# Optimization experiments

Hardware: AMD Instinct MI355X
Metric: run time of the kernel (lower is better)

## Reference

```python
import jax, jax.numpy as jnp
import numpy as np

BN = 1024      # B*N voxel groups
M = 32         # points per voxel
D_MODEL = 128
D_POINTS = 64


def _mlp(x, w1, b1, w2, b2):
    # Linear -> ReLU -> Linear (torch nn.Sequential equivalent)
    return jax.nn.relu(x @ w1 + b1) @ w2 + b2


def setup_inputs() -> dict:
    key = jax.random.key(0)
    ks = jax.random.split(key, 16)
    def lin(k, din, dout):
        return (jax.random.normal(k, (din, dout), jnp.float32) / np.sqrt(din)).astype(jnp.float32)
    inp = {}
    inp["pv_xyz"] = jax.random.normal(ks[0], (BN, M, 3), jnp.float32)
    inp["features"] = jax.random.normal(ks[1], (BN, M, D_POINTS), jnp.float32)
    i = 2
    for name, din in [("alpha", 3), ("beta", 3), ("delta", 3), ("epsilon", D_MODEL), ("omega", D_POINTS)]:
        inp[f"{name}_w1"] = lin(ks[i], din, D_MODEL); i += 1
        inp[f"{name}_b1"] = jnp.zeros((D_MODEL,), jnp.float32)
        inp[f"{name}_w2"] = lin(ks[i], D_MODEL, D_MODEL); i += 1
        inp[f"{name}_b2"] = jnp.zeros((D_MODEL,), jnp.float32)
    return inp


def reference(pv_xyz, features,
              alpha_w1, alpha_b1, alpha_w2, alpha_b2,
              beta_w1, beta_b1, beta_w2, beta_b2,
              delta_w1, delta_b1, delta_w2, delta_b2,
              epsilon_w1, epsilon_b1, epsilon_w2, epsilon_b2,
              omega_w1, omega_b1, omega_w2, omega_b2):
    # abs relative position: [BN, M, M, 3]
    dist = jnp.abs(pv_xyz[:, :, None, :] - pv_xyz[:, None, :, :])
    pij = _mlp(dist, delta_w1, delta_b1, delta_w2, delta_b2)          # [BN,M,M,D]
    q = _mlp(pv_xyz, alpha_w1, alpha_b1, alpha_w2, alpha_b2)          # [BN,M,D]
    k = _mlp(pv_xyz, beta_w1, beta_b1, beta_w2, beta_b2)              # [BN,M,D]
    v = _mlp(features, omega_w1, omega_b1, omega_w2, omega_b2)        # [BN,M,D]
    scale = jnp.float32(1.0 / np.sqrt(D_MODEL))
    w = _mlp((q[:, :, None, :] - k[:, None, :, :] + pij) * scale,
             epsilon_w1, epsilon_b1, epsilon_w2, epsilon_b2)          # [BN,M,M,D]
    wij = jax.nn.softmax(w, axis=-2)                                  # softmax over key axis
    # torch.einsum('bmmf,bmf->bmf', wij, v): repeated index -> diagonal of wij
    midx = jnp.arange(wij.shape[1])
    res = wij[:, midx, midx, :] * v                                   # [BN,M,D]
    return jnp.concatenate([res, features], axis=-1)                  # [BN,M,D+C]
```

## Files before the change

### kernel.cpp

```cpp
#include <hip/hip_runtime.h>
#include <hip/hip_bf16.h>
#include <cstdint>
#include <cstddef>


#define SCALE 0.08838834764831843f
#define LOG2E 1.4426950408889634f

typedef __bf16 bf16x8 __attribute__((ext_vector_type(8)));
typedef float f32x16 __attribute__((ext_vector_type(16)));

__device__ __forceinline__ ushort f2b(float f){
  __hip_bfloat16 h = __float2bfloat16(f);
  return __builtin_bit_cast(ushort, h);
}
__device__ __forceinline__ float b2f(uint32_t s){
  union { uint32_t u; float f; } x; x.u = s << 16; return x.f;
}
__device__ __forceinline__ float blo(uint32_t u){
  union { uint32_t x; float f; } v; v.x = u << 16; return v.f;
}
__device__ __forceinline__ float bhi(uint32_t u){
  union { uint32_t x; float f; } v; v.x = u & 0xffff0000u; return v.f;
}
__device__ __forceinline__ uint32_t pk2(float a, float b){
  union { __hip_bfloat162 h2; uint32_t u; } x;
  x.h2.x = __float2bfloat16(a); x.h2.y = __float2bfloat16(b);
  return x.u;
}
__device__ __forceinline__ f32x16 MFMA(uint4 a, uint4 b, f32x16 c){
  return __builtin_amdgcn_mfma_f32_32x32x16_bf16(
      __builtin_bit_cast(bf16x8, a), __builtin_bit_cast(bf16x8, b), c, 0, 0, 0);
}

__global__ __launch_bounds__(256) void k_pre(
    const float* __restrict__ A2, const float* __restrict__ B2, const float* __restrict__ D2,
    const float* __restrict__ E1, const float* __restrict__ E2,
    const float* __restrict__ O1, const float* __restrict__ O2,
    const float* __restrict__ ab2, const float* __restrict__ bb2, const float* __restrict__ db2,
    const float* __restrict__ eb1,
    const float* __restrict__ D1, const float* __restrict__ db1,
    ushort* __restrict__ aep, ushort* __restrict__ bep, ushort* __restrict__ gtp,
    ushort* __restrict__ e2p, ushort* __restrict__ o2p, ushort* __restrict__ o1t,
    ushort* __restrict__ d1p, float* __restrict__ c0)
{
  const int bid = blockIdx.x, tid = threadIdx.x;
  if (bid < 192){
    const float* W = (bid < 64) ? A2 : (bid < 128) ? B2 : D2;
    ushort* dst    = (bid < 64) ? aep : (bid < 128) ? bep : gtp;
    int flat = (bid & 63)*256 + tid;
    int co = flat >> 10, rem = flat & 1023, h = rem >> 3, i = rem & 7;
    int r = co*8 + i;
    float acc = 0.f;
    for (int t = 0; t < 128; ++t) acc = fmaf(W[r*128 + t], E1[t*128 + h], acc);
    dst[(co*128 + h)*8 + i] = f2b(acc * SCALE);
  } else if (bid < 256){
    int flat = (bid - 192)*256 + tid;
    int co = flat >> 10, rem = flat & 1023, d = rem >> 3, i = rem & 7;
    e2p[(co*128 + d)*8 + i] = f2b(E2[(co*8 + i)*128 + d] * LOG2E);
  } else if (bid < 320){
    int flat = (bid - 256)*256 + tid;
    int co = flat >> 10, rem = flat & 1023, d = rem >> 3, i = rem & 7;
    o2p[(co*128 + d)*8 + i] = f2b(O2[(co*8 + i)*128 + d]);
  } else if (bid < 352){
    int flat = (bid - 320)*256 + tid;
    int fo = flat >> 10, rem = flat & 1023, o = rem >> 3, e = rem & 7;
    o1t[(fo*128 + o)*8 + e] = f2b(O1[(fo*8 + e)*128 + o]);
  } else if (bid < 360){
    int flat = (bid - 352)*256 + tid;
    int koct = flat >> 10, cd = (flat >> 3) & 127, e = flat & 7;
    float val = 0.f;
    if (koct == 0){
      if (e < 3) val = D1[e*128 + cd];
      else if (e == 3) val = db1[cd];
    }
    d1p[flat] = f2b(val);
  } else {
    if (tid < 128){
      float acc = 0.f;
      for (int t = 0; t < 128; ++t) acc = fmaf(ab2[t] - bb2[t] + db2[t], E1[t*128 + tid], acc);
      c0[tid] = acc * SCALE + eb1[tid];
    }
  }
}

__device__ __forceinline__ void gemm64x128(const ushort (*sa)[64][8], const ushort (*sw)[128][8],
                                           int w, int l31, int hl, int p0,
                                           const float* __restrict__ bias,
                                           ushort* __restrict__ dst)
{
  const int rw = w >> 1, ctb = (w & 1) * 2;
  f32x16 acc0, acc1;
#pragma unroll
  for (int r = 0; r < 16; ++r){ acc0[r] = 0.f; acc1[r] = 0.f; }
#pragma unroll
  for (int kk = 0; kk < 8; ++kk){
    uint4 a  = *(const uint4*)&sa[2*kk + hl][32*rw + l31][0];
    uint4 b0 = *(const uint4*)&sw[2*kk + hl][32*ctb + l31][0];
    uint4 b1 = *(const uint4*)&sw[2*kk + hl][32*(ctb+1) + l31][0];
    acc0 = MFMA(a, b0, acc0);
    acc1 = MFMA(a, b1, acc1);
  }
#pragma unroll
  for (int t = 0; t < 2; ++t){
    const f32x16 acc = t ? acc1 : acc0;
    const int d = 32*(ctb + t) + l31;
    const float bv = bias ? bias[d] : 0.f;
#pragma unroll
    for (int r = 0; r < 16; ++r){
      int row = 32*rw + (r & 3) + 8*(r >> 2) + 4*hl;
      dst[(size_t)(p0 + row)*128 + d] = f2b(acc[r] + bv);
    }
  }
}

__global__ __launch_bounds__(256, 2) void k_point(
    const float* __restrict__ pv, const float* __restrict__ feat,
    const float* __restrict__ A1, const float* __restrict__ ab1,
    const float* __restrict__ B1, const float* __restrict__ bb1,
    const float* __restrict__ ob1, const float* __restrict__ ob2,
    const float* __restrict__ c0,
    const uint4* __restrict__ aep, const uint4* __restrict__ bep,
    const uint4* __restrict__ o1t, const uint4* __restrict__ o2p,
    ushort* __restrict__ qe_ws, ushort* __restrict__ ke_ws, ushort* __restrict__ v_ws,
    float* __restrict__ out)
{
  __shared__ ushort sW[16][128][8];
  __shared__ ushort sA[16][64][8];
  __shared__ ushort sF[8][64][8];
  __shared__ float  sLw[3][128];
  __shared__ float  sLb[128];
  __shared__ float  sLb2[128];

  const int tid = threadIdx.x;
  const int p0  = blockIdx.x * 64;
  const int w = tid >> 6, lane = tid & 63, l31 = lane & 31, hl = lane >> 5;

  for (int idx = tid; idx < 64*16; idx += 256){
    int p = idx >> 4, k4 = idx & 15;
    float4 f = ((const float4*)(feat + (size_t)(p0 + p)*64))[k4];
    ((float4*)(out + (size_t)(p0 + p)*192 + 128))[k4] = f;
  }

  for (int idx = tid; idx < 2048; idx += 256) ((uint4*)sW)[idx] = aep[idx];
  for (int idx = tid; idx < 384; idx += 256) ((float*)sLw)[idx] = A1[idx];
  if (tid < 128) sLb[tid] = ab1[tid];
  __syncthreads();
  {
    int p = tid & 63, ob = tid >> 6;
    float x0 = pv[(size_t)(p0+p)*3+0], x1 = pv[(size_t)(p0+p)*3+1], x2 = pv[(size_t)(p0+p)*3+2];
#pragma unroll
    for (int it = 0; it < 4; ++it){
      int oct = ob + 4*it;
      float h[8];
#pragma unroll
      for (int e = 0; e < 8; ++e){
        int cd = oct*8 + e;
        float t = fmaf(x0, sLw[0][cd], fmaf(x1, sLw[1][cd], fmaf(x2, sLw[2][cd], sLb[cd])));
        h[e] = fmaxf(t, 0.f);
      }
      uint4 u; u.x = pk2(h[0],h[1]); u.y = pk2(h[2],h[3]); u.z = pk2(h[4],h[5]); u.w = pk2(h[6],h[7]);
      *(uint4*)&sA[oct][p][0] = u;
    }
  }
  __syncthreads();
  gemm64x128(sA, sW, w, l31, hl, p0, c0, qe_ws);
  __syncthreads();

  for (int idx = tid; idx < 2048; idx += 256) ((uint4*)sW)[idx] = bep[idx];
  for (int idx = tid; idx < 384; idx += 256) ((float*)sLw)[idx] = B1[idx];
  if (tid < 128) sLb[tid] = bb1[tid];
  __syncthreads();
  {
    int p = tid & 63, ob = tid >> 6;
    float x0 = pv[(size_t)(p0+p)*3+0], x1 = pv[(size_t)(p0+p)*3+1], x2 = pv[(size_t)(p0+p)*3+2];
#pragma unroll
    for (int it = 0; it < 4; ++it){
      int oct = ob + 4*it;
      float h[8];
#pragma unroll
      for (int e = 0; e < 8; ++e){
        int cd = oct*8 + e;
        float t = fmaf(x0, sLw[0][cd], fmaf(x1, sLw[1][cd], fmaf(x2, sLw[2][cd], sLb[cd])));
        h[e] = fmaxf(t, 0.f);
      }
      uint4 u; u.x = pk2(h[0],h[1]); u.y = pk2(h[2],h[3]); u.z = pk2(h[4],h[5]); u.w = pk2(h[6],h[7]);
      *(uint4*)&sA[oct][p][0] = u;
    }
  }
  __syncthreads();
  gemm64x128(sA, sW, w, l31, hl, p0, nullptr, ke_ws);
  __syncthreads();

  for (int idx = tid; idx < 512; idx += 256){
    int p = idx & 63, fo = idx >> 6;
    const float* fp = feat + (size_t)(p0 + p)*64 + 8*fo;
    float4 f0 = ((const float4*)fp)[0], f1 = ((const float4*)fp)[1];
    uint4 u; u.x = pk2(f0.x,f0.y); u.y = pk2(f0.z,f0.w); u.z = pk2(f1.x,f1.y); u.w = pk2(f1.z,f1.w);
    *(uint4*)&sF[fo][p][0] = u;
  }
  for (int idx = tid; idx < 1024; idx += 256) ((uint4*)sW)[idx] = o1t[idx];
  if (tid < 128) sLb[tid] = ob1[tid];
  __syncthreads();
  {
    f32x16 acc0, acc1;
#pragma unroll
    for (int r = 0; r < 16; ++r){ acc0[r] = 0.f; acc1[r] = 0.f; }
#pragma unroll
    for (int kk = 0; kk < 4; ++kk){
      uint4 a  = *(const uint4*)&sW[2*kk + hl][32*w + l31][0];
      uint4 b0 = *(const uint4*)&sF[2*kk + hl][l31][0];
      uint4 b1 = *(const uint4*)&sF[2*kk + hl][32 + l31][0];
      acc0 = MFMA(a, b0, acc0);
      acc1 = MFMA(a, b1, acc1);
    }
#pragma unroll
    for (int t = 0; t < 2; ++t){
      const f32x16 acc = t ? acc1 : acc0;
      const int pt = 32*t + l31;
#pragma unroll
      for (int q = 0; q < 4; ++q){
        int o0 = 32*w + 8*q + 4*hl;
        float z0 = fmaxf(acc[4*q+0] + sLb[o0+0], 0.f);
        float z1 = fmaxf(acc[4*q+1] + sLb[o0+1], 0.f);
        float z2 = fmaxf(acc[4*q+2] + sLb[o0+2], 0.f);
        float z3 = fmaxf(acc[4*q+3] + sLb[o0+3], 0.f);
        uint2 u; u.x = pk2(z0, z1); u.y = pk2(z2, z3);
        *(uint2*)&sA[4*w + q][pt][4*hl] = u;
      }
    }
  }
  __syncthreads();

  for (int idx = tid; idx < 2048; idx += 256) ((uint4*)sW)[idx] = o2p[idx];
  if (tid < 128) sLb2[tid] = ob2[tid];
  __syncthreads();
  {
    const int rw = w >> 1, ctb = (w & 1) * 2;
    f32x16 acc0, acc1;
#pragma unroll
    for (int r = 0; r < 16; ++r){ acc0[r] = 0.f; acc1[r] = 0.f; }
#pragma unroll
    for (int kk = 0; kk < 8; ++kk){
      uint4 a  = *(const uint4*)&sA[2*kk + hl][32*rw + l31][0];
      uint4 b0 = *(const uint4*)&sW[2*kk + hl][32*ctb + l31][0];
      uint4 b1 = *(const uint4*)&sW[2*kk + hl][32*(ctb+1) + l31][0];
      acc0 = MFMA(a, b0, acc0);
      acc1 = MFMA(a, b1, acc1);
    }
#pragma unroll
    for (int t = 0; t < 2; ++t){
      const f32x16 acc = t ? acc1 : acc0;
      const int d = 32*(ctb + t) + l31;
      const float bias = sLb2[d];
#pragma unroll
      for (int r = 0; r < 16; ++r){
        int row = 32*rw + (r & 3) + 8*(r >> 2) + 4*hl;
        v_ws[(size_t)(p0 + row)*128 + d] = f2b(acc[r] + bias);
      }
    }
  }
}

__global__ __launch_bounds__(256, 3) void k_main(
    const float* __restrict__ pv,
    const ushort* __restrict__ qe_ws, const ushort* __restrict__ ke_ws, const ushort* __restrict__ v_ws,
    const uint4* __restrict__ gtp, const uint4* __restrict__ e2p, const uint4* __restrict__ d1p,
    float* __restrict__ out)
{
  __shared__ ushort sHDE[16][128][8];
  __shared__ float  sQE[16][128];
  __shared__ float  sXYZ[32][3];

  const int tid = threadIdx.x;
  const int b   = blockIdx.x >> 1;
  const int ch0 = (blockIdx.x & 1) * 4;
  const int w = tid >> 6, lane = tid & 63, l31 = lane & 31, hl = lane >> 5;

  for (int idx = tid; idx < 96; idx += 256) ((float*)sXYZ)[idx] = pv[(size_t)b*96 + idx];
  for (int idx = tid; idx < 512; idx += 256){
    int il = idx >> 5, sl = idx & 31;
    uint2 qu = ((const uint2*)qe_ws)[(size_t)(b*32 + 4*ch0 + il)*32 + sl];
    float4 o; o.x = blo(qu.x); o.y = bhi(qu.x); o.z = blo(qu.y); o.w = bhi(qu.y);
    ((float4*)&sQE[il][0])[sl] = o;
  }

  float kreg[16];
  {
    const ushort* kp = ke_ws + (size_t)(b*32 + l31)*128 + 32*w + 4*hl;
#pragma unroll
    for (int q = 0; q < 4; ++q){
      uint2 ku = *(const uint2*)(kp + 8*q);
      kreg[4*q+0] = blo(ku.x); kreg[4*q+1] = bhi(ku.x);
      kreg[4*q+2] = blo(ku.y); kreg[4*q+3] = bhi(ku.y);
    }
  }
  uint4 wG[8], wE[8];
#pragma unroll
  for (int kk = 0; kk < 8; ++kk){
    wG[kk] = gtp[(2*kk + hl)*128 + 32*w + l31];
    wE[kk] = e2p[(2*kk + hl)*128 + 32*w + l31];
  }
  uint4 wD = d1p[hl*128 + 32*w + l31];

  f32x16 ZERO;
#pragma unroll
  for (int r = 0; r < 16; ++r) ZERO[r] = 0.f;
  __syncthreads();

  const float xj0 = sXYZ[l31][0], xj1 = sXYZ[l31][1], xj2 = sXYZ[l31][2];

#pragma unroll
  for (int cc = 0; cc < 4; ++cc){
    const int c = ch0 + cc;

    f32x16 accD[4];
#pragma unroll
    for (int ct = 0; ct < 4; ++ct){
      const int i = 4*c + ct;
      float dx = fabsf(sXYZ[i][0] - xj0);
      float dy = fabsf(sXYZ[i][1] - xj1);
      float dz = fabsf(sXYZ[i][2] - xj2);
      uint4 bD; bD.x = pk2(dx, dy); bD.y = pk2(dz, 1.0f); bD.z = 0u; bD.w = 0u;
      accD[ct] = MFMA(wD, bD, ZERO);
    }
#pragma unroll
    for (int ct = 0; ct < 4; ++ct){
#pragma unroll
      for (int q = 0; q < 4; ++q){
        uint2 o;
        o.x = pk2(fmaxf(accD[ct][4*q+0],0.f), fmaxf(accD[ct][4*q+1],0.f));
        o.y = pk2(fmaxf(accD[ct][4*q+2],0.f), fmaxf(accD[ct][4*q+3],0.f));
        *(uint2*)&sHDE[4*w + q][32*ct + l31][4*hl] = o;
      }
    }
    __syncthreads();

    f32x16 acc1[4];
#pragma unroll
    for (int ct = 0; ct < 4; ++ct){
      const int il = 4*cc + ct;
#pragma unroll
      for (int q = 0; q < 4; ++q){
        float4 qv = *(const float4*)&sQE[il][32*w + 4*hl + 8*q];
        acc1[ct][4*q+0] = qv.x - kreg[4*q+0];
        acc1[ct][4*q+1] = qv.y - kreg[4*q+1];
        acc1[ct][4*q+2] = qv.z - kreg[4*q+2];
        acc1[ct][4*q+3] = qv.w - kreg[4*q+3];
      }
    }
#pragma unroll
    for (int kk = 0; kk < 8; ++kk){
      uint4 a = wG[kk];
#pragma unroll
      for (int ct = 0; ct < 4; ++ct){
        uint4 bu = *(const uint4*)&sHDE[2*kk + hl][32*ct + l31][0];
        acc1[ct] = MFMA(a, bu, acc1[ct]);
      }
    }
    __syncthreads();

#pragma unroll
    for (int ct = 0; ct < 4; ++ct){
#pragma unroll
      for (int q = 0; q < 4; ++q){
        uint2 o;
        o.x = pk2(fmaxf(acc1[ct][4*q+0],0.f), fmaxf(acc1[ct][4*q+1],0.f));
        o.y = pk2(fmaxf(acc1[ct][4*q+2],0.f), fmaxf(acc1[ct][4*q+3],0.f));
        *(uint2*)&sHDE[4*w + q][32*ct + l31][4*hl] = o;
      }
    }
    __syncthreads();

    float vv[4];
#pragma unroll
    for (int rt = 0; rt < 4; ++rt)
      vv[rt] = b2f((uint32_t)v_ws[(size_t)(b*32 + 4*c + rt)*128 + 32*w + l31]);

    f32x16 acc2[4];
#pragma unroll
    for (int kk = 0; kk < 8; ++kk){
      uint4 bfrag = wE[kk];
#pragma unroll
      for (int rt = 0; rt < 4; ++rt){
        uint4 au = *(const uint4*)&sHDE[2*kk + hl][32*rt + l31][0];
        acc2[rt] = MFMA(au, bfrag, kk ? acc2[rt] : ZERO);
      }
    }
    __syncthreads();

    const int g = (c >> 1) & 3;
    const int hls = c & 1;
#pragma unroll
    for (int rt = 0; rt < 4; ++rt){
      float e[16];
#pragma unroll
      for (int r = 0; r < 16; ++r) e[r] = __builtin_amdgcn_exp2f(acc2[rt][r]);
      float s01 = e[0]+e[1],   s23 = e[2]+e[3],   s45 = e[4]+e[5],   s67 = e[6]+e[7];
      float s89 = e[8]+e[9],   sab = e[10]+e[11], scd = e[12]+e[13], sef = e[14]+e[15];
      float s = ((s01+s23)+(s45+s67)) + ((s89+sab)+(scd+sef));
      s += __shfl_xor(s, 32);
      float num = (g == 0) ? e[rt] : (g == 1) ? e[rt+4] : (g == 2) ? e[rt+8] : e[rt+12];
      if (hl == hls){
        out[(size_t)(b*32 + 4*c + rt)*192 + 32*w + l31] = num * __builtin_amdgcn_rcpf(s) * vv[rt];
      }
    }
  }
}

static constexpr size_t OFF_AEP = 0;
static constexpr size_t OFF_BEP = 32768;
static constexpr size_t OFF_GTP = 65536;
static constexpr size_t OFF_E2P = 98304;
static constexpr size_t OFF_O1T = 131072;
static constexpr size_t OFF_O2P = 147456;
static constexpr size_t OFF_C0  = 180224;
static constexpr size_t OFF_D1P = 180736;
static constexpr size_t OFF_QE  = 184832;
static constexpr size_t OFF_KE  = OFF_QE + (size_t)32768*128*2;
static constexpr size_t OFF_V   = OFF_KE + (size_t)32768*128*2;

extern "C" void kernel_launch(void* const* d_in, const int* in_sizes, int n_in,
                              void* d_out, int out_size, void* d_ws, size_t ws_size,
                              hipStream_t stream)
{
  (void)in_sizes; (void)n_in; (void)out_size; (void)ws_size;
  const float* pv   = (const float*)d_in[0];
  const float* feat = (const float*)d_in[1];
  const float* A1 = (const float*)d_in[2];  const float* ab1 = (const float*)d_in[3];
  const float* A2 = (const float*)d_in[4];  const float* ab2 = (const float*)d_in[5];
  const float* B1 = (const float*)d_in[6];  const float* bb1 = (const float*)d_in[7];
  const float* B2 = (const float*)d_in[8];  const float* bb2 = (const float*)d_in[9];
  const float* D1 = (const float*)d_in[10]; const float* db1 = (const float*)d_in[11];
  const float* D2 = (const float*)d_in[12]; const float* db2 = (const float*)d_in[13];
  const float* E1 = (const float*)d_in[14]; const float* eb1 = (const float*)d_in[15];
  const float* E2 = (const float*)d_in[16];
  const float* O1 = (const float*)d_in[18]; const float* ob1 = (const float*)d_in[19];
  const float* O2 = (const float*)d_in[20]; const float* ob2 = (const float*)d_in[21];

  char* ws = (char*)d_ws;
  ushort* aep = (ushort*)(ws + OFF_AEP);
  ushort* bep = (ushort*)(ws + OFF_BEP);
  ushort* gtp = (ushort*)(ws + OFF_GTP);
  ushort* e2p = (ushort*)(ws + OFF_E2P);
  ushort* o1t = (ushort*)(ws + OFF_O1T);
  ushort* o2p = (ushort*)(ws + OFF_O2P);
  float*  c0  = (float*)(ws + OFF_C0);
  ushort* d1p = (ushort*)(ws + OFF_D1P);
  ushort* qe  = (ushort*)(ws + OFF_QE);
  ushort* ke  = (ushort*)(ws + OFF_KE);
  ushort* vv  = (ushort*)(ws + OFF_V);
  float* out = (float*)d_out;

  hipLaunchKernelGGL(k_pre, dim3(361), dim3(256), 0, stream,
                     A2, B2, D2, E1, E2, O1, O2, ab2, bb2, db2, eb1, D1, db1,
                     aep, bep, gtp, e2p, o2p, o1t, d1p, c0);
  hipLaunchKernelGGL(k_point, dim3(512), dim3(256), 0, stream,
                     pv, feat, A1, ab1, B1, bb1, ob1, ob2, c0,
                     (const uint4*)aep, (const uint4*)bep, (const uint4*)o1t, (const uint4*)o2p,
                     qe, ke, vv, out);
  hipLaunchKernelGGL(k_main, dim3(2048), dim3(256), 0, stream,
                     pv, qe, ke, vv, (const uint4*)gtp, (const uint4*)e2p, (const uint4*)d1p,
                     out);
}
```

Before: 118.7 us.

## Keep MLP intermediates in registers via permlane swaps instead of LDS round-trips

Restructures k_main so each wave owns two query rows at a time. The MFMA accumulator-to-operand layout conversion now happens in registers with permlane32_swap, replacing the shared-memory staging of hidden activations and its block-wide barriers. Weights G and E are moved from per-lane registers into LDS, the grid is halved to one block per voxel group, and the occupancy hint drops from 3 to 2. The cost is many more LDS weight reads per MFMA and higher register pressure, traded for removing all in-loop __syncthreads.

Result: no change. 120.1 us (+1.2%).

```diff
diff --git a/kernel.cpp b/kernel.cpp
--- a/kernel.cpp
+++ b/kernel.cpp
@@ -9,6 +9,7 @@
 
 typedef __bf16 bf16x8 __attribute__((ext_vector_type(8)));
 typedef float f32x16 __attribute__((ext_vector_type(16)));
+typedef unsigned int u32x2 __attribute__((ext_vector_type(2)));
 
 __device__ __forceinline__ ushort f2b(float f){
   __hip_bfloat16 h = __float2bfloat16(f);
@@ -31,6 +32,33 @@
 __device__ __forceinline__ f32x16 MFMA(uint4 a, uint4 b, f32x16 c){
   return __builtin_amdgcn_mfma_f32_32x32x16_bf16(
       __builtin_bit_cast(bf16x8, a), __builtin_bit_cast(bf16x8, b), c, 0, 0, 0);
+}
+
+__device__ __forceinline__ uint2 pswap(uint32_t a, uint32_t b){
+#if __has_builtin(__builtin_amdgcn_permlane32_swap)
+  u32x2 r = __builtin_amdgcn_permlane32_swap(a, b, false, false);
+  uint2 o; o.x = r[0]; o.y = r[1]; return o;
+#else
+  uint32_t am = (uint32_t)__shfl_xor((int)a, 32);
+  uint32_t bm = (uint32_t)__shfl_xor((int)b, 32);
+  bool hi = (threadIdx.x & 32) != 0;
+  uint2 o; o.x = hi ? bm : a; o.y = hi ? b : am; return o;
+#endif
+}
+
+__device__ __forceinline__ void packswap(const f32x16 c, uint4& f0, uint4& f1){
+  uint32_t p01 = pk2(fmaxf(c[0],0.f),  fmaxf(c[1],0.f));
+  uint32_t p23 = pk2(fmaxf(c[2],0.f),  fmaxf(c[3],0.f));
+  uint32_t p45 = pk2(fmaxf(c[4],0.f),  fmaxf(c[5],0.f));
+  uint32_t p67 = pk2(fmaxf(c[6],0.f),  fmaxf(c[7],0.f));
+  uint32_t p89 = pk2(fmaxf(c[8],0.f),  fmaxf(c[9],0.f));
+  uint32_t pab = pk2(fmaxf(c[10],0.f), fmaxf(c[11],0.f));
+  uint32_t pcd = pk2(fmaxf(c[12],0.f), fmaxf(c[13],0.f));
+  uint32_t pef = pk2(fmaxf(c[14],0.f), fmaxf(c[15],0.f));
+  uint2 s0 = pswap(p01, p45), s1 = pswap(p23, p67);
+  uint2 s2 = pswap(p89, pcd), s3 = pswap(pab, pef);
+  f0.x = s0.x; f0.y = s1.x; f0.z = s0.y; f0.w = s1.y;
+  f1.x = s2.x; f1.y = s3.x; f1.z = s2.y; f1.w = s3.y;
 }
 
 __global__ __launch_bounds__(256) void k_pre(
@@ -262,147 +290,119 @@
   }
 }
 
-__global__ __launch_bounds__(256, 3) void k_main(
+__global__ __launch_bounds__(256, 2) void k_main(
     const float* __restrict__ pv,
     const ushort* __restrict__ qe_ws, const ushort* __restrict__ ke_ws, const ushort* __restrict__ v_ws,
     const uint4* __restrict__ gtp, const uint4* __restrict__ e2p, const uint4* __restrict__ d1p,
     float* __restrict__ out)
 {
-  __shared__ ushort sHDE[16][128][8];
-  __shared__ float  sQE[16][128];
-  __shared__ float  sXYZ[32][3];
+  __shared__ uint4 sG[2048];
+  __shared__ uint4 sE[2048];
+  __shared__ uint2 sK[1024];
+  __shared__ float sXYZ[32][3];
 
   const int tid = threadIdx.x;
-  const int b   = blockIdx.x >> 1;
-  const int ch0 = (blockIdx.x & 1) * 4;
+  const int b = blockIdx.x;
   const int w = tid >> 6, lane = tid & 63, l31 = lane & 31, hl = lane >> 5;
 
+  for (int idx = tid; idx < 2048; idx += 256){ sG[idx] = gtp[idx]; sE[idx] = e2p[idx]; }
+  for (int idx = tid; idx < 1024; idx += 256){
+    int j = idx & 31, rest = idx >> 5;
+    int khl = rest & 1, slot = rest >> 1;
+    int h0 = 32*(slot >> 2) + 8*(slot & 3) + 4*khl;
+    sK[idx] = *(const uint2*)(ke_ws + (size_t)(b*32 + j)*128 + h0);
+  }
   for (int idx = tid; idx < 96; idx += 256) ((float*)sXYZ)[idx] = pv[(size_t)b*96 + idx];
-  for (int idx = tid; idx < 512; idx += 256){
-    int il = idx >> 5, sl = idx & 31;
-    uint2 qu = ((const uint2*)qe_ws)[(size_t)(b*32 + 4*ch0 + il)*32 + sl];
-    float4 o; o.x = blo(qu.x); o.y = bhi(qu.x); o.z = blo(qu.y); o.w = bhi(qu.y);
-    ((float4*)&sQE[il][0])[sl] = o;
-  }
-
-  float kreg[16];
-  {
-    const ushort* kp = ke_ws + (size_t)(b*32 + l31)*128 + 32*w + 4*hl;
-#pragma unroll
-    for (int q = 0; q < 4; ++q){
-      uint2 ku = *(const uint2*)(kp + 8*q);
-      kreg[4*q+0] = blo(ku.x); kreg[4*q+1] = bhi(ku.x);
-      kreg[4*q+2] = blo(ku.y); kreg[4*q+3] = bhi(ku.y);
-    }
-  }
-  uint4 wG[8], wE[8];
-#pragma unroll
-  for (int kk = 0; kk < 8; ++kk){
-    wG[kk] = gtp[(2*kk + hl)*128 + 32*w + l31];
-    wE[kk] = e2p[(2*kk + hl)*128 + 32*w + l31];
-  }
-  uint4 wD = d1p[hl*128 + 32*w + l31];
-
+
+  uint4 wD[4];
+#pragma unroll
+  for (int t = 0; t < 4; ++t) wD[t] = d1p[hl*128 + 32*t + l31];
   f32x16 ZERO;
 #pragma unroll
   for (int r = 0; r < 16; ++r) ZERO[r] = 0.f;
   __syncthreads();
 
   const float xj0 = sXYZ[l31][0], xj1 = sXYZ[l31][1], xj2 = sXYZ[l31][2];
-
-#pragma unroll
-  for (int cc = 0; cc < 4; ++cc){
-    const int c = ch0 + cc;
-
-    f32x16 accD[4];
-#pragma unroll
-    for (int ct = 0; ct < 4; ++ct){
-      const int i = 4*c + ct;
-      float dx = fabsf(sXYZ[i][0] - xj0);
-      float dy = fabsf(sXYZ[i][1] - xj1);
-      float dz = fabsf(sXYZ[i][2] - xj2);
-      uint4 bD; bD.x = pk2(dx, dy); bD.y = pk2(dz, 1.0f); bD.z = 0u; bD.w = 0u;
-      accD[ct] = MFMA(wD, bD, ZERO);
-    }
-#pragma unroll
-    for (int ct = 0; ct < 4; ++ct){
+  const ushort* qbase = qe_ws + (size_t)b*32*128;
+
+#pragma unroll
+  for (int pp = 0; pp < 4; ++pp){
+    const int i0 = 8*w + 2*pp, i1 = i0 + 1;
+
+    uint4 bDa, bDb;
+    {
+      float a0 = sXYZ[i0][0], a1 = sXYZ[i0][1], a2 = sXYZ[i0][2];
+      float c0_ = sXYZ[i1][0], c1_ = sXYZ[i1][1], c2_ = sXYZ[i1][2];
+      bDa.x = pk2(fabsf(a0-xj0), fabsf(a1-xj1)); bDa.y = pk2(fabsf(a2-xj2), 1.0f);
+      bDa.z = 0u; bDa.w = 0u;
+      bDb.x = pk2(fabsf(c0_-xj0), fabsf(c1_-xj1)); bDb.y = pk2(fabsf(c2_-xj2), 1.0f);
+      bDb.z = 0u; bDb.w = 0u;
+    }
+
+    uint4 hdA[8], hdB[8];
+#pragma unroll
+    for (int t = 0; t < 4; ++t){
+      f32x16 ca = MFMA(wD[t], bDa, ZERO);
+      f32x16 cb = MFMA(wD[t], bDb, ZERO);
+      packswap(ca, hdA[2*t], hdA[2*t+1]);
+      packswap(cb, hdB[2*t], hdB[2*t+1]);
+    }
+
+    uint4 heA[8], heB[8];
+#pragma unroll
+    for (int t = 0; t < 4; ++t){
+      f32x16 aA, aB;
 #pragma unroll
       for (int q = 0; q < 4; ++q){
-        uint2 o;
-        o.x = pk2(fmaxf(accD[ct][4*q+0],0.f), fmaxf(accD[ct][4*q+1],0.f));
-        o.y = pk2(fmaxf(accD[ct][4*q+2],0.f), fmaxf(accD[ct][4*q+3],0.f));
-        *(uint2*)&sHDE[4*w + q][32*ct + l31][4*hl] = o;
-      }
-    }
-    __syncthreads();
-
-    f32x16 acc1[4];
-#pragma unroll
-    for (int ct = 0; ct < 4; ++ct){
-      const int il = 4*cc + ct;
-#pragma unroll
-      for (int q = 0; q < 4; ++q){
-        float4 qv = *(const float4*)&sQE[il][32*w + 4*hl + 8*q];
-        acc1[ct][4*q+0] = qv.x - kreg[4*q+0];
-        acc1[ct][4*q+1] = qv.y - kreg[4*q+1];
-        acc1[ct][4*q+2] = qv.z - kreg[4*q+2];
-        acc1[ct][4*q+3] = qv.w - kreg[4*q+3];
-      }
-    }
-#pragma unroll
-    for (int kk = 0; kk < 8; ++kk){
-      uint4 a = wG[kk];
-#pragma unroll
-      for (int ct = 0; ct < 4; ++ct){
-        uint4 bu = *(const uint4*)&sHDE[2*kk + hl][32*ct + l31][0];
-        acc1[ct] = MFMA(a, bu, acc1[ct]);
-      }
-    }
-    __syncthreads();
-
-#pragma unroll
-    for (int ct = 0; ct < 4; ++ct){
-#pragma unroll
-      for (int q = 0; q < 4; ++q){
-        uint2 o;
-        o.x = pk2(fmaxf(acc1[ct][4*q+0],0.f), fmaxf(acc1[ct][4*q+1],0.f));
-        o.y = pk2(fmaxf(acc1[ct][4*q+2],0.f), fmaxf(acc1[ct][4*q+3],0.f));
-        *(uint2*)&sHDE[4*w + q][32*ct + l31][4*hl] = o;
-      }
-    }
-    __syncthreads();
-
-    float vv[4];
-#pragma unroll
-    for (int rt = 0; rt < 4; ++rt)
-      vv[rt] = b2f((uint32_t)v_ws[(size_t)(b*32 + 4*c + rt)*128 + 32*w + l31]);
-
-    f32x16 acc2[4];
-#pragma unroll
-    for (int kk = 0; kk < 8; ++kk){
-      uint4 bfrag = wE[kk];
-#pragma unroll
-      for (int rt = 0; rt < 4; ++rt){
-        uint4 au = *(const uint4*)&sHDE[2*kk + hl][32*rt + l31][0];
-        acc2[rt] = MFMA(au, bfrag, kk ? acc2[rt] : ZERO);
-      }
-    }
-    __syncthreads();
-
-    const int g = (c >> 1) & 3;
-    const int hls = c & 1;
-#pragma unroll
-    for (int rt = 0; rt < 4; ++rt){
-      float e[16];
-#pragma unroll
-      for (int r = 0; r < 16; ++r) e[r] = __builtin_amdgcn_exp2f(acc2[rt][r]);
-      float s01 = e[0]+e[1],   s23 = e[2]+e[3],   s45 = e[4]+e[5],   s67 = e[6]+e[7];
-      float s89 = e[8]+e[9],   sab = e[10]+e[11], scd = e[12]+e[13], sef = e[14]+e[15];
-      float s = ((s01+s23)+(s45+s67)) + ((s89+sab)+(scd+sef));
-      s += __shfl_xor(s, 32);
-      float num = (g == 0) ? e[rt] : (g == 1) ? e[rt+4] : (g == 2) ? e[rt+8] : e[rt+12];
-      if (hl == hls){
-        out[(size_t)(b*32 + 4*c + rt)*192 + 32*w + l31] = num * __builtin_amdgcn_rcpf(s) * vv[rt];
+        uint2 kq = sK[((t*4 + q)*2 + hl)*32 + l31];
+        uint2 qa = *(const uint2*)(qbase + (size_t)i0*128 + 32*t + 8*q + 4*hl);
+        uint2 qb = *(const uint2*)(qbase + (size_t)i1*128 + 32*t + 8*q + 4*hl);
+        float k0 = blo(kq.x), k1 = bhi(kq.x), k2 = blo(kq.y), k3 = bhi(kq.y);
+        aA[4*q+0] = blo(qa.x) - k0; aA[4*q+1] = bhi(qa.x) - k1;
+        aA[4*q+2] = blo(qa.y) - k2; aA[4*q+3] = bhi(qa.y) - k3;
+        aB[4*q+0] = blo(qb.x) - k0; aB[4*q+1] = bhi(qb.x) - k1;
+        aB[4*q+2] = blo(qb.y) - k2; aB[4*q+3] = bhi(qb.y) - k3;
+      }
+#pragma unroll
+      for (int kk = 0; kk < 8; ++kk){
+        uint4 wg = sG[(2*kk + hl)*128 + 32*t + l31];
+        aA = MFMA(wg, hdA[kk], aA);
+        aB = MFMA(wg, hdB[kk], aB);
+      }
+      packswap(aA, heA[2*t], heA[2*t+1]);
+      packswap(aB, heB[2*t], heB[2*t+1]);
+    }
+
+    const int rl   = (2*pp) & 3;
+    const int hsel = pp >> 1;
+#pragma unroll
+    for (int t = 0; t < 4; ++t){
+      float va = b2f((uint32_t)v_ws[(size_t)(b*32 + i0)*128 + 32*t + l31]);
+      float vb = b2f((uint32_t)v_ws[(size_t)(b*32 + i1)*128 + 32*t + l31]);
+      f32x16 cA, cB;
+#pragma unroll
+      for (int kk = 0; kk < 8; ++kk){
+        uint4 we = sE[(2*kk + hl)*128 + 32*t + l31];
+        cA = MFMA(heA[kk], we, kk ? cA : ZERO);
+        cB = MFMA(heB[kk], we, kk ? cB : ZERO);
+      }
+#pragma unroll
+      for (int r = 0; r < 16; ++r) cA[r] = __builtin_amdgcn_exp2f(cA[r]);
+#pragma unroll
+      for (int r = 0; r < 16; ++r) cB[r] = __builtin_amdgcn_exp2f(cB[r]);
+      float sA = ((cA[0]+cA[1])+(cA[2]+cA[3])) + ((cA[4]+cA[5])+(cA[6]+cA[7]))
+               + ((cA[8]+cA[9])+(cA[10]+cA[11])) + ((cA[12]+cA[13])+(cA[14]+cA[15]));
+      float sB = ((cB[0]+cB[1])+(cB[2]+cB[3])) + ((cB[4]+cB[5])+(cB[6]+cB[7]))
+               + ((cB[8]+cB[9])+(cB[10]+cB[11])) + ((cB[12]+cB[13])+(cB[14]+cB[15]));
+      uint2 swA = pswap(__builtin_bit_cast(uint32_t, sA), __builtin_bit_cast(uint32_t, sA));
+      uint2 swB = pswap(__builtin_bit_cast(uint32_t, sB), __builtin_bit_cast(uint32_t, sB));
+      float sAt = __builtin_bit_cast(float, swA.x) + __builtin_bit_cast(float, swA.y);
+      float sBt = __builtin_bit_cast(float, swB.x) + __builtin_bit_cast(float, swB.y);
+      float nA = (w == 0) ? cA[rl]   : (w == 1) ? cA[rl+4]   : (w == 2) ? cA[rl+8]   : cA[rl+12];
+      float nB = (w == 0) ? cB[rl+1] : (w == 1) ? cB[rl+5]   : (w == 2) ? cB[rl+9]   : cB[rl+13];
+      if (hl == hsel){
+        out[(size_t)(b*32 + i0)*192 + 32*t + l31] = nA * __builtin_amdgcn_rcpf(sAt) * va;
+        out[(size_t)(b*32 + i1)*192 + 32*t + l31] = nB * __builtin_amdgcn_rcpf(sBt) * vb;
       }
     }
   }
@@ -459,7 +459,7 @@
                      pv, feat, A1, ab1, B1, bb1, ob1, ob2, c0,
                      (const uint4*)aep, (const uint4*)bep, (const uint4*)o1t, (const uint4*)o2p,
                      qe, ke, vv, out);
-  hipLaunchKernelGGL(k_main, dim3(2048), dim3(256), 0, stream,
+  hipLaunchKernelGGL(k_main, dim3(1024), dim3(256), 0, stream,
                      pv, qe, ke, vv, (const uint4*)gtp, (const uint4*)e2p, (const uint4*)d1p,
                      out);
 }
```
